# Kernel optimization log

Hardware: AMD Instinct MI355X
Metric: run time of the kernel (lower is better)

## Reference

```python
import jax, jax.numpy as jnp
import numpy as np

N_NODES = 50000


def setup_inputs() -> dict:
    key = jax.random.key(0)
    ks = jax.random.split(key, 5)
    d_in, d_out = 512, 512
    n_edges = 800000
    x = jax.random.normal(ks[0], (N_NODES, d_in), dtype=jnp.float32)
    edge_index = jax.random.randint(ks[1], (2, n_edges), 0, N_NODES, dtype=jnp.int64)
    s = 1.0 / np.sqrt(d_in)
    W_l = jax.random.uniform(ks[2], (d_out, d_in), dtype=jnp.float32, minval=-s, maxval=s)
    b_l = jax.random.uniform(ks[3], (d_out,), dtype=jnp.float32, minval=-s, maxval=s)
    W_r = jax.random.uniform(ks[4], (d_out, d_in), dtype=jnp.float32, minval=-s, maxval=s)
    return {"x": x, "edge_index": edge_index, "W_l": W_l, "b_l": b_l, "W_r": W_r}


def reference(x, edge_index, W_l, b_l, W_r):
    # lin_l: dense transform before aggregation
    x_l = x @ W_l.T + b_l                       # [N, d_out]
    src, dst = edge_index[0], edge_index[1]
    # sparse adjacency matmul (SAGE mean-neighbor aggregation):
    # out_l[i] = mean_{j in N(i)} x_l[j]
    agg = jax.ops.segment_sum(x_l[src], dst, num_segments=N_NODES)   # [N, d_out]
    deg = jax.ops.segment_sum(jnp.ones_like(src, dtype=x.dtype), dst,
                              num_segments=N_NODES)                  # [N]
    out_l = agg / jnp.maximum(deg, 1.0)[:, None]
    # lin_r: self-loop transform (no bias)
    out_r = x @ W_r.T
    return out_l + out_r
```

## Files before the change

kernel.cpp:

```cpp
#include <hip/hip_runtime.h>

typedef __bf16 bf16x8 __attribute__((ext_vector_type(8)));
typedef float floatx4 __attribute__((ext_vector_type(4)));
typedef float floatx2 __attribute__((ext_vector_type(2)));
typedef unsigned short ushortx8 __attribute__((ext_vector_type(8)));

__device__ __forceinline__ unsigned short f2b(float f) {
    union { float f; unsigned u; } v; v.f = f;
    unsigned r = v.u + 0x7fffu + ((v.u >> 16) & 1u);
    return (unsigned short)(r >> 16);
}


__global__ void deg_count_kernel(const int* __restrict__ dst, int* __restrict__ deg, int nE) {
    int e = blockIdx.x * blockDim.x + threadIdx.x;
    if (e < nE) atomicAdd(&deg[dst[e]], 1);
}

__global__ void scan1_kernel(const int* __restrict__ deg, int* __restrict__ bsum, int n) {
    __shared__ int s[256];
    int b = blockIdx.x, t = threadIdx.x;
    int base = b * 1024 + t * 4;
    int v = 0;
#pragma unroll
    for (int i = 0; i < 4; i++) { int idx = base + i; if (idx < n) v += deg[idx]; }
    s[t] = v; __syncthreads();
    for (int o = 128; o > 0; o >>= 1) { if (t < o) s[t] += s[t + o]; __syncthreads(); }
    if (t == 0) bsum[b] = s[0];
}

__global__ void scan3_kernel(const int* __restrict__ deg, const int* __restrict__ bsum,
                             int* __restrict__ off, int n, int nb, int nE) {
    __shared__ int s[256];
    __shared__ int base_s;
    int b = blockIdx.x, t = threadIdx.x;
    if (t < 64) {
        int v = (t < nb && t < b) ? bsum[t] : 0;
        for (int o = 32; o > 0; o >>= 1) v += __shfl_down(v, o, 64);
        if (t == 0) base_s = v;
    }
    int idx = b * 1024 + t * 4;
    int a0 = (idx     < n) ? deg[idx]     : 0;
    int a1 = (idx + 1 < n) ? deg[idx + 1] : 0;
    int a2 = (idx + 2 < n) ? deg[idx + 2] : 0;
    int a3 = (idx + 3 < n) ? deg[idx + 3] : 0;
    int tsum = a0 + a1 + a2 + a3;
    s[t] = tsum; __syncthreads();
    for (int o = 1; o < 256; o <<= 1) {
        int u = (t >= o) ? s[t - o] : 0;
        __syncthreads();
        s[t] += u;
        __syncthreads();
    }
    int excl = s[t] - tsum + base_s;
    if (idx     < n) off[idx]     = excl;
    if (idx + 1 < n) off[idx + 1] = excl + a0;
    if (idx + 2 < n) off[idx + 2] = excl + a0 + a1;
    if (idx + 3 < n) off[idx + 3] = excl + a0 + a1 + a2;
    if (b == 0 && t == 0) off[n] = nE;
}

__global__ void fill_kernel(const int* __restrict__ src, const int* __restrict__ dst,
                            const int* __restrict__ off, int* __restrict__ cursor,
                            int* __restrict__ csr, int nE) {
    int e = blockIdx.x * blockDim.x + threadIdx.x;
    if (e < nE) {
        int d = dst[e];
        int pos = atomicAdd(&cursor[d], 1);
        csr[off[d] + pos] = src[e];
    }
}


__global__ void conv_kernel(const float* __restrict__ x, unsigned short* __restrict__ Abuf,
                            unsigned char* __restrict__ X8,
                            const float* __restrict__ Wl, const float* __restrict__ Wr,
                            unsigned short* __restrict__ Wcat,
                            int Mreal, long nx) {
    long t = (long)blockIdx.x * blockDim.x + threadIdx.x;
    if (t < nx) {
        long row = t >> 6;
        int c8 = (int)(t & 63) * 8;
        if (row < Mreal) {
            const float4* p4 = (const float4*)(x + row * 512 + c8);
            float4 v0 = p4[0], v1 = p4[1];
            ushortx8 o8;
            o8[0] = f2b(v0.x); o8[1] = f2b(v0.y); o8[2] = f2b(v0.z); o8[3] = f2b(v0.w);
            o8[4] = f2b(v1.x); o8[5] = f2b(v1.y); o8[6] = f2b(v1.z); o8[7] = f2b(v1.w);
            *(ushortx8*)(Abuf + row * 1024 + 512 + c8) = o8;
            unsigned int pa = __builtin_amdgcn_cvt_pk_fp8_f32(v0.x, v0.y, 0, false);
            pa = __builtin_amdgcn_cvt_pk_fp8_f32(v0.z, v0.w, pa, true);
            unsigned int pb = __builtin_amdgcn_cvt_pk_fp8_f32(v1.x, v1.y, 0, false);
            pb = __builtin_amdgcn_cvt_pk_fp8_f32(v1.z, v1.w, pb, true);
            *(uint2*)(X8 + row * 512 + c8) = make_uint2(pa, pb);
        } else {
            ushortx8 z = {0, 0, 0, 0, 0, 0, 0, 0};
            *(ushortx8*)(Abuf + row * 1024 + c8) = z;
            *(ushortx8*)(Abuf + row * 1024 + 512 + c8) = z;
        }
    } else {
        long u = t - nx;
        if (u >= 65536) return;
        int o = (int)(u >> 7);
        int c8 = (int)(u & 127) * 8;
        const float* p = (c8 < 512) ? (Wl + o * 512 + c8) : (Wr + o * 512 + (c8 - 512));
        float4 v0 = ((const float4*)p)[0], v1 = ((const float4*)p)[1];
        ushortx8 o8;
        o8[0] = f2b(v0.x); o8[1] = f2b(v0.y); o8[2] = f2b(v0.z); o8[3] = f2b(v0.w);
        o8[4] = f2b(v1.x); o8[5] = f2b(v1.y); o8[6] = f2b(v1.z); o8[7] = f2b(v1.w);
        *(ushortx8*)(Wcat + (long)o * 1024 + c8) = o8;
    }
}


__global__ void agg_kernel(const unsigned char* __restrict__ X8,
                           const int* __restrict__ off, const int* __restrict__ csr,
                           unsigned short* __restrict__ Abuf_w, int n) {
    int wid = (int)((blockIdx.x * (long)blockDim.x + threadIdx.x) >> 6);
    int l = threadIdx.x & 63;
    if (wid >= n) return;
    int beg = off[wid], end = off[wid + 1];
    float a[8] = {};
    int e = beg;
    while (e < end) {
        int cnt = end - e; if (cnt > 64) cnt = 64;
        int myi = csr[e + (l < cnt ? l : cnt - 1)];
        int s0 = __builtin_amdgcn_readlane(myi, 0);
        uint2 p = *(const uint2*)(X8 + (long)s0 * 512 + l * 8);
        for (int j = 1; j < cnt; j++) {
            int s = __builtin_amdgcn_readlane(myi, j);
            uint2 pn = *(const uint2*)(X8 + (long)s * 512 + l * 8);
            floatx2 f0 = __builtin_amdgcn_cvt_pk_f32_fp8(p.x, false);
            floatx2 f1 = __builtin_amdgcn_cvt_pk_f32_fp8(p.x, true);
            floatx2 f2 = __builtin_amdgcn_cvt_pk_f32_fp8(p.y, false);
            floatx2 f3 = __builtin_amdgcn_cvt_pk_f32_fp8(p.y, true);
            a[0] += f0[0]; a[1] += f0[1]; a[2] += f1[0]; a[3] += f1[1];
            a[4] += f2[0]; a[5] += f2[1]; a[6] += f3[0]; a[7] += f3[1];
            p = pn;
        }
        {
            floatx2 f0 = __builtin_amdgcn_cvt_pk_f32_fp8(p.x, false);
            floatx2 f1 = __builtin_amdgcn_cvt_pk_f32_fp8(p.x, true);
            floatx2 f2 = __builtin_amdgcn_cvt_pk_f32_fp8(p.y, false);
            floatx2 f3 = __builtin_amdgcn_cvt_pk_f32_fp8(p.y, true);
            a[0] += f0[0]; a[1] += f0[1]; a[2] += f1[0]; a[3] += f1[1];
            a[4] += f2[0]; a[5] += f2[1]; a[6] += f3[0]; a[7] += f3[1];
        }
        e += cnt;
    }
    int d = end - beg;
    float inv = 1.0f / (float)(d > 0 ? d : 1);
    ushortx8 o8;
#pragma unroll
    for (int i = 0; i < 8; i++) o8[i] = f2b(a[i] * inv);
    *(ushortx8*)(Abuf_w + (long)wid * 1024 + l * 8) = o8;
}


__global__ __launch_bounds__(256, 3)
void gemm_kernel(const unsigned short* __restrict__ A, const unsigned short* __restrict__ B,
                 const float* __restrict__ bl, const int* __restrict__ deg,
                 float* __restrict__ out, int Mreal, int nby) {
    int L = blockIdx.x;
    int by = (L >> 5) * 8 + (L & 7);
    int bx = (L >> 3) & 3;
    if (by >= nby) return;

    __shared__ unsigned short As[128 * 32];
    __shared__ unsigned short Bs[128 * 32];
    int tid = threadIdx.x;
    int w = tid >> 6, l = tid & 63;
    long i0 = (long)by * 128;
    int n0 = bx * 128;
    int wm = (w >> 1) * 64, wn = (w & 1) * 64;
    int r = l & 15, q = l >> 4;
    int srow = l >> 2;
    int sch = (l & 3) * 8;

    floatx4 acc[4][4] = {};

    for (int k0 = 0; k0 < 1024; k0 += 32) {
#pragma unroll
        for (int j = 0; j < 2; j++) {
            int s = w * 2 + j;
            int row = s * 16 + srow;
            const unsigned short* ga = A + (i0 + row) * 1024 + k0 + sch;
            const unsigned short* gb = B + (long)(n0 + row) * 1024 + k0 + sch;
            __builtin_amdgcn_global_load_lds(
                (__attribute__((address_space(1))) void*)(uintptr_t)ga,
                (__attribute__((address_space(3))) void*)(uintptr_t)(As + s * 512), 16, 0, 0);
            __builtin_amdgcn_global_load_lds(
                (__attribute__((address_space(1))) void*)(uintptr_t)gb,
                (__attribute__((address_space(3))) void*)(uintptr_t)(Bs + s * 512), 16, 0, 0);
        }
        __syncthreads();
        bf16x8 af[4], bfr[4];
#pragma unroll
        for (int a = 0; a < 4; a++)
            af[a] = *(const bf16x8*)(As + (wm + a * 16 + r) * 32 + q * 8);
#pragma unroll
        for (int b = 0; b < 4; b++)
            bfr[b] = *(const bf16x8*)(Bs + (wn + b * 16 + r) * 32 + q * 8);
#pragma unroll
        for (int a = 0; a < 4; a++)
#pragma unroll
            for (int b = 0; b < 4; b++)
                acc[a][b] = __builtin_amdgcn_mfma_f32_16x16x32_bf16(af[a], bfr[b], acc[a][b], 0, 0, 0);
        __syncthreads();
    }

#pragma unroll
    for (int a = 0; a < 4; a++) {
        long rb = i0 + wm + a * 16 + q * 4;
#pragma unroll
        for (int rr = 0; rr < 4; rr++) {
            long row = rb + rr;
            if (row < Mreal) {
                bool hasdeg = deg[row] > 0;
#pragma unroll
                for (int b = 0; b < 4; b++) {
                    int col = n0 + wn + b * 16 + r;
                    float v = acc[a][b][rr];
                    if (hasdeg) v += bl[col];
                    out[row * 512 + col] = v;
                }
            }
        }
    }
}


extern "C" void kernel_launch(void* const* d_in, const int* in_sizes, int n_in,
                              void* d_out, int out_size, void* d_ws, size_t ws_size,
                              hipStream_t stream) {
    const float* x  = (const float*)d_in[0];
    const int* eidx = (const int*)d_in[1];
    const float* Wl = (const float*)d_in[2];
    const float* bl = (const float*)d_in[3];
    const float* Wr = (const float*)d_in[4];
    float* out = (float*)d_out;

    int N  = in_sizes[0] / 512;
    int nE = in_sizes[1] / 2;
    const int* src = eidx;
    const int* dst = eidx + nE;
    int Mpad = (N + 127) & ~127;
    int nb = (N + 1023) / 1024;
    int nby = Mpad / 128;

    char* w = (char*)d_ws;
    size_t o = 0;
    auto alloc = [&](size_t bytes) { void* p = w + o; o = (o + bytes + 255) & ~255UL; return p; };
    int* deg    = (int*)alloc((size_t)N * 4);
    int* cursor = (int*)alloc((size_t)N * 4);
    int* off    = (int*)alloc((size_t)(N + 1) * 4);
    int* bsum   = (int*)alloc((size_t)nb * 4);
    int* csr    = (int*)alloc((size_t)nE * 4);
    unsigned short* Wcat = (unsigned short*)alloc((size_t)512 * 1024 * 2);
    unsigned short* Abuf = (unsigned short*)alloc((size_t)Mpad * 1024 * 2);
    unsigned char*  X8   = (unsigned char*)alloc((size_t)Mpad * 512);
    if (o > ws_size) return;

    hipMemsetAsync(deg, 0, (size_t)N * 4, stream);
    hipMemsetAsync(cursor, 0, (size_t)N * 4, stream);

    deg_count_kernel<<<(nE + 255) / 256, 256, 0, stream>>>(dst, deg, nE);
    scan1_kernel<<<nb, 256, 0, stream>>>(deg, bsum, N);
    scan3_kernel<<<nb, 256, 0, stream>>>(deg, bsum, off, N, nb, nE);
    fill_kernel<<<(nE + 255) / 256, 256, 0, stream>>>(src, dst, off, cursor, csr, nE);
    long nx = (long)Mpad * 64;
    conv_kernel<<<(int)((nx + 65536 + 255) / 256), 256, 0, stream>>>(x, Abuf, X8, Wl, Wr, Wcat, N, nx);
    agg_kernel<<<(N * 64 + 255) / 256, 256, 0, stream>>>(X8, off, csr, Abuf, N);

    int nbyp = (nby + 7) & ~7;
    gemm_kernel<<<nbyp * 4, 256, 0, stream>>>(Abuf, Wcat, bl, deg, out, N, nby);
}
```

Baseline: 417.3 us.

## Double-buffer GEMM LDS tiles with XOR swizzle and deepen aggregation prefetch

The GEMM now keeps two LDS buffers, so the next K tile is loaded while MFMAs run on the current one. The global source column is XOR-swizzled by row so that LDS fragment reads avoid bank conflicts. The aggregation kernel now prefetches four neighbor rows at a time instead of one, which puts more gather loads in flight. Doubling LDS to 32KB per block may lower occupancy under launch_bounds(256,3), and the swizzle has to match exactly between the writes and the reads.

```diff
diff --git a/kernel.cpp b/kernel.cpp
--- a/kernel.cpp
+++ b/kernel.cpp
@@ -113,6 +113,20 @@
 }
 
 
+__device__ __forceinline__ uint2 ldrow(const unsigned char* __restrict__ X8, int myi, int idx, int l) {
+    int s = __builtin_amdgcn_readlane(myi, idx);
+    return *(const uint2*)(X8 + (long)s * 512 + l * 8);
+}
+
+__device__ __forceinline__ void accum(float* a, uint2 p) {
+    floatx2 f0 = __builtin_amdgcn_cvt_pk_f32_fp8(p.x, false);
+    floatx2 f1 = __builtin_amdgcn_cvt_pk_f32_fp8(p.x, true);
+    floatx2 f2 = __builtin_amdgcn_cvt_pk_f32_fp8(p.y, false);
+    floatx2 f3 = __builtin_amdgcn_cvt_pk_f32_fp8(p.y, true);
+    a[0] += f0[0]; a[1] += f0[1]; a[2] += f1[0]; a[3] += f1[1];
+    a[4] += f2[0]; a[5] += f2[1]; a[6] += f3[0]; a[7] += f3[1];
+}
+
 __global__ void agg_kernel(const unsigned char* __restrict__ X8,
                            const int* __restrict__ off, const int* __restrict__ csr,
                            unsigned short* __restrict__ Abuf_w, int n) {
@@ -125,27 +139,25 @@
     while (e < end) {
         int cnt = end - e; if (cnt > 64) cnt = 64;
         int myi = csr[e + (l < cnt ? l : cnt - 1)];
-        int s0 = __builtin_amdgcn_readlane(myi, 0);
-        uint2 p = *(const uint2*)(X8 + (long)s0 * 512 + l * 8);
-        for (int j = 1; j < cnt; j++) {
-            int s = __builtin_amdgcn_readlane(myi, j);
-            uint2 pn = *(const uint2*)(X8 + (long)s * 512 + l * 8);
-            floatx2 f0 = __builtin_amdgcn_cvt_pk_f32_fp8(p.x, false);
-            floatx2 f1 = __builtin_amdgcn_cvt_pk_f32_fp8(p.x, true);
-            floatx2 f2 = __builtin_amdgcn_cvt_pk_f32_fp8(p.y, false);
-            floatx2 f3 = __builtin_amdgcn_cvt_pk_f32_fp8(p.y, true);
-            a[0] += f0[0]; a[1] += f0[1]; a[2] += f1[0]; a[3] += f1[1];
-            a[4] += f2[0]; a[5] += f2[1]; a[6] += f3[0]; a[7] += f3[1];
-            p = pn;
-        }
-        {
-            floatx2 f0 = __builtin_amdgcn_cvt_pk_f32_fp8(p.x, false);
-            floatx2 f1 = __builtin_amdgcn_cvt_pk_f32_fp8(p.x, true);
-            floatx2 f2 = __builtin_amdgcn_cvt_pk_f32_fp8(p.y, false);
-            floatx2 f3 = __builtin_amdgcn_cvt_pk_f32_fp8(p.y, true);
-            a[0] += f0[0]; a[1] += f0[1]; a[2] += f1[0]; a[3] += f1[1];
-            a[4] += f2[0]; a[5] += f2[1]; a[6] += f3[0]; a[7] += f3[1];
-        }
+        int c1 = cnt - 1;
+        uint2 b0 = ldrow(X8, myi, 0, l);
+        uint2 b1 = ldrow(X8, myi, 1 < c1 ? 1 : c1, l);
+        uint2 b2 = ldrow(X8, myi, 2 < c1 ? 2 : c1, l);
+        uint2 b3 = ldrow(X8, myi, 3 < c1 ? 3 : c1, l);
+        int j = 0;
+        for (; j + 4 < cnt; j += 4) {
+            uint2 n0 = ldrow(X8, myi, j + 4, l);
+            uint2 n1 = ldrow(X8, myi, j + 5 < c1 ? j + 5 : c1, l);
+            uint2 n2 = ldrow(X8, myi, j + 6 < c1 ? j + 6 : c1, l);
+            uint2 n3 = ldrow(X8, myi, j + 7 < c1 ? j + 7 : c1, l);
+            accum(a, b0); accum(a, b1); accum(a, b2); accum(a, b3);
+            b0 = n0; b1 = n1; b2 = n2; b3 = n3;
+        }
+        int rem = cnt - j;
+        accum(a, b0);
+        if (rem > 1) accum(a, b1);
+        if (rem > 2) accum(a, b2);
+        if (rem > 3) accum(a, b3);
         e += cnt;
     }
     int d = end - beg;
@@ -166,8 +178,8 @@
     int bx = (L >> 3) & 3;
     if (by >= nby) return;
 
-    __shared__ unsigned short As[128 * 32];
-    __shared__ unsigned short Bs[128 * 32];
+    __shared__ unsigned short As[2][128 * 32];
+    __shared__ unsigned short Bs[2][128 * 32];
     int tid = threadIdx.x;
     int w = tid >> 6, l = tid & 63;
     long i0 = (long)by * 128;
@@ -175,32 +187,40 @@
     int wm = (w >> 1) * 64, wn = (w & 1) * 64;
     int r = l & 15, q = l >> 4;
     int srow = l >> 2;
-    int sch = (l & 3) * 8;
+    int cg8 = ((l & 3) ^ ((srow >> 1) & 3)) * 8;
+    int p8 = (q ^ ((r >> 1) & 3)) * 8;
 
     floatx4 acc[4][4] = {};
 
-    for (int k0 = 0; k0 < 1024; k0 += 32) {
+    auto stage = [&](int buf, int k0) {
 #pragma unroll
         for (int j = 0; j < 2; j++) {
             int s = w * 2 + j;
             int row = s * 16 + srow;
-            const unsigned short* ga = A + (i0 + row) * 1024 + k0 + sch;
-            const unsigned short* gb = B + (long)(n0 + row) * 1024 + k0 + sch;
+            const unsigned short* ga = A + (i0 + row) * 1024 + k0 + cg8;
+            const unsigned short* gb = B + (long)(n0 + row) * 1024 + k0 + cg8;
             __builtin_amdgcn_global_load_lds(
                 (__attribute__((address_space(1))) void*)(uintptr_t)ga,
-                (__attribute__((address_space(3))) void*)(uintptr_t)(As + s * 512), 16, 0, 0);
+                (__attribute__((address_space(3))) void*)(uintptr_t)(&As[buf][s * 512]), 16, 0, 0);
             __builtin_amdgcn_global_load_lds(
                 (__attribute__((address_space(1))) void*)(uintptr_t)gb,
-                (__attribute__((address_space(3))) void*)(uintptr_t)(Bs + s * 512), 16, 0, 0);
-        }
-        __syncthreads();
+                (__attribute__((address_space(3))) void*)(uintptr_t)(&Bs[buf][s * 512]), 16, 0, 0);
+        }
+    };
+
+    stage(0, 0);
+    __syncthreads();
+
+    for (int t = 0; t < 32; t++) {
+        int cur = t & 1;
+        if (t < 31) stage(cur ^ 1, (t + 1) * 32);
         bf16x8 af[4], bfr[4];
 #pragma unroll
         for (int a = 0; a < 4; a++)
-            af[a] = *(const bf16x8*)(As + (wm + a * 16 + r) * 32 + q * 8);
+            af[a] = *(const bf16x8*)(&As[cur][(wm + a * 16 + r) * 32 + p8]);
 #pragma unroll
         for (int b = 0; b < 4; b++)
-            bfr[b] = *(const bf16x8*)(Bs + (wn + b * 16 + r) * 32 + q * 8);
+            bfr[b] = *(const bf16x8*)(&Bs[cur][(wn + b * 16 + r) * 32 + p8]);
 #pragma unroll
         for (int a = 0; a < 4; a++)
 #pragma unroll
```

Result: faster. 405.5 us (-2.8%).
